# Kernel optimization log

Hardware: AMD Instinct MI355X
Metric: run time of the kernel (lower is better)

## Reference

```python
import jax, jax.numpy as jnp
import numpy as np

VOCAB = 50000
DIM = 50
B = 131072
CTX = 10
NEG = 10
EPS = 1e-10


def setup_inputs() -> dict:
    key = jax.random.key(0)
    k1, k2, k3, k4, k5 = jax.random.split(key, 5)
    return {
        "context_idxs": jax.random.randint(k1, (B, CTX), 0, VOCAB),
        "pos_target": jax.random.randint(k2, (B,), 0, VOCAB),
        "neg_samples": jax.random.randint(k3, (B, NEG), 0, VOCAB),
        "in_embed_W": jax.random.normal(k4, (VOCAB, DIM), dtype=jnp.float32),
        "out_embed_W": jax.random.normal(k5, (VOCAB, DIM), dtype=jnp.float32),
    }


def reference(context_idxs, pos_target, neg_samples, in_embed_W, out_embed_W):
    # context_vec: [B, D] = mean over context window of in_embed gathers
    context_vec = in_embed_W[context_idxs].mean(axis=1)
    # positive score: [B]
    pos_embeds = out_embed_W[pos_target]                      # [B, D]
    pos_score = jnp.sum(context_vec * pos_embeds, axis=1)     # [B]
    pos_loss = jnp.log(jax.nn.sigmoid(pos_score) + EPS)       # [B]
    # negative scores: [B, K] = bmm(neg_embeds [B,K,D], context_vec [B,D,1])
    neg_embeds = out_embed_W[neg_samples]                     # [B, K, D]
    neg_score = jnp.einsum("bkd,bd->bk", neg_embeds, context_vec)
    neg_loss = jnp.log(jax.nn.sigmoid(-neg_score) + EPS).sum(axis=1)  # [B]
    return -(pos_loss + neg_loss).mean()
```

## Files before the change

kernel.cpp:

```cpp
#include <hip/hip_runtime.h>
#include <hip/hip_fp8.h>

#define VOCAB 50000
#define DIM   50
#define B_TOT 131072
#define CTX   10
#define NEG   10
#define EPS_F 1e-10f
#define PAIRS (B_TOT / 2)

constexpr int TPB    = 256;
constexpr int BLOCKS = 2048;
constexpr int NWAVES = BLOCKS * (TPB / 64);
constexpr int ITERS  = PAIRS / NWAVES;
static_assert(PAIRS % NWAVES == 0, "exact division required");

constexpr size_t ROW8_B  = 64;
constexpr size_t TAB8_B  = (size_t)VOCAB * ROW8_B;
constexpr size_t WS_NEED = 2 * TAB8_B + BLOCKS * 4;

constexpr int BUF_W = 48 * 16;

typedef float vf2 __attribute__((ext_vector_type(2)));

static __device__ __forceinline__ void fp8x8_to_f32x8(unsigned long long w,
                                                      float* f) {
#if __has_builtin(__builtin_amdgcn_cvt_pk_f32_fp8)
    const int lo = (int)(unsigned int)w;
    const int hi = (int)(unsigned int)(w >> 32);
    vf2 a = __builtin_amdgcn_cvt_pk_f32_fp8(lo, false);
    vf2 b = __builtin_amdgcn_cvt_pk_f32_fp8(lo, true);
    vf2 c = __builtin_amdgcn_cvt_pk_f32_fp8(hi, false);
    vf2 d = __builtin_amdgcn_cvt_pk_f32_fp8(hi, true);
    f[0] = a[0]; f[1] = a[1]; f[2] = b[0]; f[3] = b[1];
    f[4] = c[0]; f[5] = c[1]; f[6] = d[0]; f[7] = d[1];
#else
    #pragma unroll
    for (int i = 0; i < 8; ++i) {
        __hip_fp8_e4m3 v;
        v.__x = (unsigned char)(w >> (8 * i));
        f[i] = (float)v;
    }
#endif
}

static __device__ __forceinline__ float dpp_add_x1(float x) {
    const int y = __builtin_amdgcn_mov_dpp(__float_as_int(x), 0xB1, 0xF, 0xF, true);
    return x + __int_as_float(y);
}
static __device__ __forceinline__ float dpp_add_x2(float x) {
    const int y = __builtin_amdgcn_mov_dpp(__float_as_int(x), 0x4E, 0xF, 0xF, true);
    return x + __int_as_float(y);
}

__global__ __launch_bounds__(256) void cbow_convert(
    const float* __restrict__ inW, const float* __restrict__ outW,
    unsigned short* __restrict__ ws8)
{
    const int t = blockIdx.x * 256 + threadIdx.x;
    const int per_tab = VOCAB * 32;
    if (t >= 2 * per_tab) return;
    const int tab = t / per_tab;
    const int rem = t - tab * per_tab;
    const int r   = rem >> 5;
    const int j   = rem & 31;

    unsigned short u = 0;
    if (j < 25) {
        const float2* src2 = (const float2*)(tab ? outW : inW);
        const float2  v    = src2[r * 25 + j];
#if __has_builtin(__builtin_amdgcn_cvt_pk_fp8_f32)
        const int pk = __builtin_amdgcn_cvt_pk_fp8_f32(v.x, v.y, 0, false);
        u = (unsigned short)(pk & 0xffff);
#else
        __hip_fp8_e4m3 a(v.x), b(v.y);
        u = (unsigned short)(a.__x | (b.__x << 8));
#endif
    }
    ws8[(size_t)tab * (VOCAB * 32) + (size_t)r * 32 + j] = u;
}

__global__ __launch_bounds__(TPB, 8) void cbow_loss_fp8(
    const int* __restrict__ ctx_idx,
    const int* __restrict__ pos_idx,
    const int* __restrict__ neg_idx,
    const unsigned short* __restrict__ ws8,
    float* __restrict__ partials)
{
    __shared__ unsigned int lds[(TPB / 64) * BUF_W];

    const int lane = threadIdx.x & 63;
    const int sub  = lane >> 5;
    const int l    = lane & 31;
    const int quad = lane >> 2;
    const int qb   = (lane & 3) * 16;
    const int g    = (l >> 3) & 3;
    const int j    = l & 7;

    const int wave  = threadIdx.x >> 6;
    unsigned int* wbase = lds + wave * BUF_W;
    const int gwave = blockIdx.x * (TPB / 64) + wave;

    const char* in8  = (const char*)ws8;
    const char* out8 = (const char*)(ws8 + (size_t)VOCAB * 32);

    auto idx_addr = [&](int b) -> const int* {
        if (l < CTX)           return ctx_idx + b * CTX + l;
        if (l == CTX)          return pos_idx + b;
        if (l < CTX + 1 + NEG) return neg_idx + b * NEG + (l - CTX - 1);
        return pos_idx + b;
    };

    float loss_lane = 0.f;

    int my_idx = *idx_addr(2 * gwave + sub);

    #pragma unroll
    for (int i = 0; i < ITERS; ++i) {
        #pragma unroll
        for (int t = 0; t < 3; ++t) {
            const int row    = t * 16 + quad;
            const int sample = (row >= 24) ? 1 : 0;
            int slot = row - sample * 24;
            slot = (slot > 20) ? 20 : slot;
            const int idx = __shfl(my_idx, sample * 32 + slot);
            const char* tb = (slot < CTX) ? in8 : out8;
            const char* ga = tb + ((size_t)(unsigned)idx << 6) + qb;
            __builtin_amdgcn_global_load_lds(
                (const __attribute__((address_space(1))) unsigned int*)ga,
                (__attribute__((address_space(3))) unsigned int*)(wbase + t * 256),
                16, 0, 0);
        }

        const int np = (i + 1 < ITERS) ? gwave + (i + 1) * NWAVES : gwave;
        const int next_idx = *idx_addr(2 * np + sub);

        asm volatile("s_waitcnt vmcnt(0)" ::: "memory");

        const char* smp = (const char*)wbase + sub * (24 * 64);

        float cv[8] = {0.f, 0.f, 0.f, 0.f, 0.f, 0.f, 0.f, 0.f};
        #pragma unroll
        for (int s = 0; s < CTX; ++s) {
            const unsigned long long w =
                *(const unsigned long long*)(smp + s * 64 + j * 8);
            float f[8];
            fp8x8_to_f32x8(w, f);
            #pragma unroll
            for (int d = 0; d < 8; ++d) cv[d] += f[d];
        }

        #pragma unroll
        for (int p = 0; p < 3; ++p) {
            const int slotr = 10 + 4 * p + g;
            const unsigned long long w =
                *(const unsigned long long*)(smp + slotr * 64 + j * 8);
            float f[8];
            fp8x8_to_f32x8(w, f);
            float prod = 0.f;
            #pragma unroll
            for (int d = 0; d < 8; ++d) prod = fmaf(cv[d], f[d], prod);
            prod = dpp_add_x1(prod);
            prod = dpp_add_x2(prod);
            prod += __shfl_xor(prod, 4);

            const bool valid = (j == 0) && !(p == 2 && g == 3);
            const float sc   = prod * (1.f / CTX);
            const float z    = (p == 0 && g == 0) ? sc : -sc;
            const float sig  = 1.f / (1.f + __expf(-z));
            const float c    = __logf(sig + EPS_F);
            loss_lane += valid ? c : 0.f;
        }

        my_idx = next_idx;
    }

    loss_lane += __shfl_xor(loss_lane, 1);
    loss_lane += __shfl_xor(loss_lane, 2);
    loss_lane += __shfl_xor(loss_lane, 4);
    loss_lane += __shfl_xor(loss_lane, 8);
    loss_lane += __shfl_xor(loss_lane, 16);
    loss_lane += __shfl_xor(loss_lane, 32);

    __shared__ float s_part[TPB / 64];
    if (lane == 0) s_part[wave] = loss_lane;
    __syncthreads();
    if (threadIdx.x == 0) {
        float s = 0.f;
        #pragma unroll
        for (int w = 0; w < TPB / 64; ++w) s += s_part[w];
        partials[blockIdx.x] = s;
    }
}

__global__ __launch_bounds__(TPB) void cbow_loss_f32(
    const int*   __restrict__ ctx_idx, const int* __restrict__ pos_idx,
    const int*   __restrict__ neg_idx, const float* __restrict__ inW,
    const float* __restrict__ outW,    float* __restrict__ partials)
{
    const int lane = threadIdx.x & 63;
    const int sub  = lane >> 5;
    const int l    = lane & 31;
    const int p    = (l < 25) ? l : 24;
    const bool act = (l < 25);
    const int wave   = threadIdx.x >> 6;
    const int gwave  = blockIdx.x * (TPB / 64) + wave;
    const float2* inW2  = (const float2*)inW;
    const float2* outW2 = (const float2*)outW;

    float loss_lane = 0.f;
    for (int pair = gwave; pair < PAIRS; pair += NWAVES) {
        const int b = 2 * pair + sub;
        float cvx = 0.f, cvy = 0.f;
        #pragma unroll
        for (int jj = 0; jj < CTX; ++jj) {
            const float2 v = inW2[ctx_idx[b * CTX + jj] * 25 + p];
            cvx += v.x; cvy += v.y;
        }
        cvx *= (1.f / CTX); cvy *= (1.f / CTX);
        float packed = 0.f;
        #pragma unroll
        for (int r = 0; r <= NEG; ++r) {
            const int idx = (r == 0) ? pos_idx[b] : neg_idx[b * NEG + r - 1];
            const float2 v = outW2[idx * 25 + p];
            float prod = act ? (cvx * v.x + cvy * v.y) : 0.f;
            prod += __shfl_xor(prod, 1);
            prod += __shfl_xor(prod, 2);
            prod += __shfl_xor(prod, 4);
            prod += __shfl_xor(prod, 8);
            prod += __shfl_xor(prod, 16);
            packed = (l == r) ? prod : packed;
        }
        const float z   = (l == 0) ? packed : -packed;
        const float sig = 1.f / (1.f + __expf(-z));
        loss_lane += (l < NEG + 1) ? __logf(sig + EPS_F) : 0.f;
    }
    loss_lane += __shfl_xor(loss_lane, 1);
    loss_lane += __shfl_xor(loss_lane, 2);
    loss_lane += __shfl_xor(loss_lane, 4);
    loss_lane += __shfl_xor(loss_lane, 8);
    loss_lane += __shfl_xor(loss_lane, 16);
    loss_lane += __shfl_xor(loss_lane, 32);
    __shared__ float s_part[TPB / 64];
    if (lane == 0) s_part[wave] = loss_lane;
    __syncthreads();
    if (threadIdx.x == 0) {
        float s = 0.f;
        #pragma unroll
        for (int w = 0; w < TPB / 64; ++w) s += s_part[w];
        partials[blockIdx.x] = s;
    }
}

__global__ __launch_bounds__(256) void cbow_finalize(
    const float* __restrict__ partials, float* __restrict__ out)
{
    float s = 0.f;
    for (int i = threadIdx.x; i < BLOCKS; i += 256) s += partials[i];
    #pragma unroll
    for (int k = 32; k >= 1; k >>= 1) s += __shfl_xor(s, k);
    __shared__ float sm[4];
    const int w = threadIdx.x >> 6;
    if ((threadIdx.x & 63) == 0) sm[w] = s;
    __syncthreads();
    if (threadIdx.x == 0)
        out[0] = -(sm[0] + sm[1] + sm[2] + sm[3]) * (1.f / (float)B_TOT);
}

extern "C" void kernel_launch(void* const* d_in, const int* in_sizes, int n_in,
                              void* d_out, int out_size, void* d_ws, size_t ws_size,
                              hipStream_t stream) {
    const int*   ctx_idx = (const int*)  d_in[0];
    const int*   pos_idx = (const int*)  d_in[1];
    const int*   neg_idx = (const int*)  d_in[2];
    const float* inW     = (const float*)d_in[3];
    const float* outW    = (const float*)d_in[4];
    float*       out     = (float*)d_out;

    if (ws_size >= WS_NEED) {
        unsigned short* ws8 = (unsigned short*)d_ws;
        float* partials = (float*)((char*)d_ws + 2 * TAB8_B);
        const int conv_threads = 2 * VOCAB * 32;
        cbow_convert<<<(conv_threads + 255) / 256, 256, 0, stream>>>(inW, outW, ws8);
        cbow_loss_fp8<<<BLOCKS, TPB, 0, stream>>>(ctx_idx, pos_idx, neg_idx, ws8, partials);
        cbow_finalize<<<1, 256, 0, stream>>>(partials, out);
    } else {
        float* partials = (float*)d_ws;
        cbow_loss_f32<<<BLOCKS, TPB, 0, stream>>>(ctx_idx, pos_idx, neg_idx, inW, outW, partials);
        cbow_finalize<<<1, 256, 0, stream>>>(partials, out);
    }
}
```

Baseline: 134.6 us.

## Pack rows densely, split context sum across lane groups, use DPP reductions

Shrinks each sample's LDS slot layout from 24 to 21 rows and skips the padding row loads for the upper lanes of the third load. The context-vector accumulation is split so each lane group sums half the context rows, then the halves are combined with a DPP row shift. The shfl_xor in the dot-product reduction becomes a DPP broadcast, and the grid is doubled to 4096 blocks. This cuts redundant loads, LDS reads and cross-lane shuffle latency, at the cost of more blocks with fewer iterations each. It also relies on the DPP control codes combining the right lanes.

```diff
diff --git a/kernel.cpp b/kernel.cpp
--- a/kernel.cpp
+++ b/kernel.cpp
@@ -10,7 +10,7 @@
 #define PAIRS (B_TOT / 2)
 
 constexpr int TPB    = 256;
-constexpr int BLOCKS = 2048;
+constexpr int BLOCKS = 4096;
 constexpr int NWAVES = BLOCKS * (TPB / 64);
 constexpr int ITERS  = PAIRS / NWAVES;
 static_assert(PAIRS % NWAVES == 0, "exact division required");
@@ -44,12 +44,9 @@
 #endif
 }
 
-static __device__ __forceinline__ float dpp_add_x1(float x) {
-    const int y = __builtin_amdgcn_mov_dpp(__float_as_int(x), 0xB1, 0xF, 0xF, true);
-    return x + __int_as_float(y);
-}
-static __device__ __forceinline__ float dpp_add_x2(float x) {
-    const int y = __builtin_amdgcn_mov_dpp(__float_as_int(x), 0x4E, 0xF, 0xF, true);
+template <int CTRL>
+static __device__ __forceinline__ float dpp_add(float x) {
+    const int y = __builtin_amdgcn_mov_dpp(__float_as_int(x), CTRL, 0xF, 0xF, true);
     return x + __int_as_float(y);
 }
 
@@ -119,17 +116,19 @@
     for (int i = 0; i < ITERS; ++i) {
         #pragma unroll
         for (int t = 0; t < 3; ++t) {
-            const int row    = t * 16 + quad;
-            const int sample = (row >= 24) ? 1 : 0;
-            int slot = row - sample * 24;
-            slot = (slot > 20) ? 20 : slot;
+            const int row  = t * 16 + quad;
+            const int crow = (row > 41) ? 41 : row;
+            const int sample = (crow >= 21) ? 1 : 0;
+            const int slot   = crow - 21 * sample;
             const int idx = __shfl(my_idx, sample * 32 + slot);
-            const char* tb = (slot < CTX) ? in8 : out8;
-            const char* ga = tb + ((size_t)(unsigned)idx << 6) + qb;
-            __builtin_amdgcn_global_load_lds(
-                (const __attribute__((address_space(1))) unsigned int*)ga,
-                (__attribute__((address_space(3))) unsigned int*)(wbase + t * 256),
-                16, 0, 0);
+            if (t < 2 || lane < 40) {
+                const char* tb = (slot < CTX) ? in8 : out8;
+                const char* ga = tb + ((size_t)(unsigned)idx << 6) + qb;
+                __builtin_amdgcn_global_load_lds(
+                    (const __attribute__((address_space(1))) unsigned int*)ga,
+                    (__attribute__((address_space(3))) unsigned int*)(wbase + t * 256),
+                    16, 0, 0);
+            }
         }
 
         const int np = (i + 1 < ITERS) ? gwave + (i + 1) * NWAVES : gwave;
@@ -137,32 +136,36 @@
 
         asm volatile("s_waitcnt vmcnt(0)" ::: "memory");
 
-        const char* smp = (const char*)wbase + sub * (24 * 64);
+        const char* smp = (const char*)wbase + sub * (21 * 64);
 
         float cv[8] = {0.f, 0.f, 0.f, 0.f, 0.f, 0.f, 0.f, 0.f};
         #pragma unroll
-        for (int s = 0; s < CTX; ++s) {
+        for (int s = 0; s < 5; ++s) {
+            const int r = (g & 1) * 5 + s;
             const unsigned long long w =
-                *(const unsigned long long*)(smp + s * 64 + j * 8);
+                *(const unsigned long long*)(smp + r * 64 + j * 8);
             float f[8];
             fp8x8_to_f32x8(w, f);
             #pragma unroll
             for (int d = 0; d < 8; ++d) cv[d] += f[d];
         }
+        #pragma unroll
+        for (int d = 0; d < 8; ++d) cv[d] = dpp_add<0x128>(cv[d]);
 
         #pragma unroll
         for (int p = 0; p < 3; ++p) {
-            const int slotr = 10 + 4 * p + g;
+            int r = 10 + 4 * p + g;
+            r = (r > 20) ? 20 : r;
             const unsigned long long w =
-                *(const unsigned long long*)(smp + slotr * 64 + j * 8);
+                *(const unsigned long long*)(smp + r * 64 + j * 8);
             float f[8];
             fp8x8_to_f32x8(w, f);
             float prod = 0.f;
             #pragma unroll
             for (int d = 0; d < 8; ++d) prod = fmaf(cv[d], f[d], prod);
-            prod = dpp_add_x1(prod);
-            prod = dpp_add_x2(prod);
-            prod += __shfl_xor(prod, 4);
+            prod = dpp_add<0xB1>(prod);
+            prod = dpp_add<0x4E>(prod);
+            prod = dpp_add<0x141>(prod);
 
             const bool valid = (j == 0) && !(p == 2 && g == 3);
             const float sc   = prod * (1.f / CTX);
```

Result: faster. 121.5 us (-9.7%).
